# Optimization experiments

Measured on AMD Instinct MI355X. Metric: run time of the kernel, lower is better.

The kernel has to match this reference:

```python
import jax, jax.numpy as jnp
import numpy as np

N = 8192        # num_nodes
H = 128         # h_dim
E = 131072      # num edges (avg degree 16)
NREL = 90       # num relations
NB = 8          # num_bases (block-diagonal decomposition)
SI = H // NB    # block size 16


def setup_inputs() -> dict:
    key = jax.random.key(0)
    ks = jax.random.split(key, 24)
    sc = 0.01
    n = lambda k, shape, s=sc: jax.random.normal(k, shape, dtype=jnp.float32) * s
    return {
        'node_ids': jnp.arange(N, dtype=jnp.int32),
        'src': jax.random.randint(ks[0], (E,), 0, N, dtype=jnp.int32),
        'dst': jax.random.randint(ks[1], (E,), 0, N, dtype=jnp.int32),
        'etypes': jax.random.randint(ks[2], (E,), 0, NREL, dtype=jnp.int32),
        'norm': jax.random.uniform(ks[3], (E, 1), dtype=jnp.float32),
        'eps': jax.random.normal(ks[4], (N, H), dtype=jnp.float32),
        # input embedding layer
        'embedding': n(ks[5], (N, H)),
        # RelGraphConv layer 0 ('bdd'): per-relation block-diag weights, self-loop, bias
        'W0': n(ks[6], (NREL, NB, SI, SI)),
        'loop0': n(ks[7], (H, H)),
        'b0': jnp.zeros((H,), jnp.float32),
        # RelGraphConv layer 1
        'W1': n(ks[8], (NREL, NB, SI, SI)),
        'loop1': n(ks[9], (H, H)),
        'b1': jnp.zeros((H,), jnp.float32),
        # z_layer: Linear(H, 2H)  (weights stored as (in, out))
        'Wz': n(ks[10], (H, 2 * H)),
        'bz': jnp.zeros((2 * H,), jnp.float32),
        # inter_layer (UpdateLayer): Linear(H, H) + h_bias
        'Wi': n(ks[11], (H, H)),
        'bi': jnp.zeros((H,), jnp.float32),
        'hbi': jnp.zeros((H,), jnp.float32),
        # output_layer (second UpdateLayer)
        'Wo': n(ks[12], (H, H)),
        'bo': jnp.zeros((H,), jnp.float32),
        'hbo': jnp.zeros((H,), jnp.float32),
    }


def _rgcn_bdd(h, W, loop_w, bias, src, dst, etypes, norm, act):
    # gather src features, split into NB blocks of size SI
    x = h[src].reshape(-1, NB, SI)                       # [E, NB, SI]
    Wg = W[etypes]                                       # [E, NB, SI, SI] per-edge relation block weights
    msg = jnp.einsum('ebi,ebio->ebo', x, Wg).reshape(-1, H) * norm  # [E, H]
    agg = jax.ops.segment_sum(msg, dst, num_segments=N)  # scatter-add to dst
    out = agg + bias + h @ loop_w                        # self-loop + bias
    return act(out) if act is not None else out


def reference(node_ids, src, dst, etypes, norm, eps, embedding,
              W0, loop0, b0, W1, loop1, b1,
              Wz, bz, Wi, bi, hbi, Wo, bo, hbo):
    # input layer: embedding lookup; saved as input_embed
    x0 = embedding[node_ids]                             # [N, H]
    h = _rgcn_bdd(x0, W0, loop0, b0, src, dst, etypes, norm, jax.nn.relu)
    h = _rgcn_bdd(h, W1, loop1, b1, src, dst, etypes, norm, None)
    # VAE head: z ~ N(mean, exp(log_std))
    zml = h @ Wz + bz                                    # [N, 2H]
    z_mean, z_log_std = jnp.split(zml, 2, axis=-1)
    z = z_mean + jnp.exp(z_log_std) * eps                # reparameterized sample
    # decode 1: outer-product reconstruction + fused update
    R = z @ z.T                                          # [N, N]
    h = R @ (z @ Wi + bi) + R @ x0 + hbi
    # decode 2
    R2 = h @ h.T                                         # [N, N]
    out = R2 @ (h @ Wo + bo) + R2 @ x0 + hbo
    return out
```

## Files before the change

### kernel.cpp

```cpp
#include <hip/hip_runtime.h>
#include <hip/hip_bf16.h>
#include <math.h>

#define Hdim 128
#define NBq 8
#define SIq 16

typedef __attribute__((ext_vector_type(8))) short short8x;
typedef __attribute__((ext_vector_type(4))) float f32x4;

__device__ inline unsigned short f2b(float f) {
  unsigned int u = __float_as_uint(f);
  return (unsigned short)((u + 0x7fffu + ((u >> 16) & 1u)) >> 16);
}
__device__ inline unsigned int pack2(float lo, float hi) {
  return (unsigned int)f2b(lo) | ((unsigned int)f2b(hi) << 16);
}

__global__ __launch_bounds__(256) void k_pre(
    const float* __restrict__ emb, const int* __restrict__ ids, float* __restrict__ x0,
    const float* __restrict__ W0, unsigned short* __restrict__ Wt0,
    const float* __restrict__ W1, unsigned short* __restrict__ Wt1, int w0elems,
    const float* __restrict__ l0, const float* __restrict__ l1,
    const float* __restrict__ Wi, const float* __restrict__ Wo, const float* __restrict__ Wz,
    unsigned short* __restrict__ l0t, unsigned short* __restrict__ l1t,
    unsigned short* __restrict__ Wit, unsigned short* __restrict__ Wot,
    unsigned short* __restrict__ Wzt,
    const int* __restrict__ dst, int* __restrict__ cnt, int E,
    int b1, int b2, int b3) {
  int bx = blockIdx.x, t = threadIdx.x;
  if (bx < b1) {
    int idx = bx * 256 + t;
    int n = idx >> 5, c4 = idx & 31;
    int s = ids[n];
    ((float4*)x0)[(size_t)n * 32 + c4] = ((const float4*)emb)[(size_t)s * 32 + c4];
  } else if (bx < b2) {
    int idx = (bx - b1) * 256 + t;
    const float* W = (idx < w0elems) ? W0 : W1;
    unsigned short* Wt = (idx < w0elems) ? Wt0 : Wt1;
    int local = (idx < w0elems) ? idx : idx - w0elems;
    int rb = local >> 8, io = local & 255;
    int i = io >> 4, o = io & 15;
    Wt[(size_t)rb * 256 + o * 16 + i] = f2b(W[(size_t)rb * 256 + i * 16 + o]);
  } else if (bx < b3) {
    int idx = (bx - b2) * 256 + t;
    if (idx < 65536) {
      int w = idx >> 14, local = idx & 16383;
      const float* in = (w == 0) ? l0 : (w == 1) ? l1 : (w == 2) ? Wi : Wo;
      unsigned short* out = (w == 0) ? l0t : (w == 1) ? l1t : (w == 2) ? Wit : Wot;
      int n = local >> 7, k = local & 127;
      out[local] = f2b(in[k * 128 + n]);
    } else {
      int local = idx - 65536;
      int n = local >> 7, k = local & 127;
      Wzt[local] = f2b(Wz[k * 256 + n]);
    }
  } else {
    int e = (bx - b3) * 256 + t;
    if (e < E) atomicAdd(&cnt[dst[e]], 1);
  }
}

__global__ __launch_bounds__(1024) void k_scan(const int* __restrict__ cnt,
                                               int* __restrict__ off,
                                               int* __restrict__ cur, int N, int E) {
  __shared__ int part[1024];
  int t = threadIdx.x;
  int ipt = N / 1024;
  int base = t * ipt;
  int loc[8];
  int s = 0;
  for (int i = 0; i < ipt; ++i) { loc[i] = s; s += cnt[base + i]; }
  part[t] = s;
  __syncthreads();
  for (int d = 1; d < 1024; d <<= 1) {
    int v = part[t];
    int add = (t >= d) ? part[t - d] : 0;
    __syncthreads();
    part[t] = v + add;
    __syncthreads();
  }
  int pre = (t == 0) ? 0 : part[t - 1];
  for (int i = 0; i < ipt; ++i) {
    int o = pre + loc[i];
    off[base + i] = o;
    cur[base + i] = o;
  }
  if (t == 0) off[N] = E;
}

__global__ void k_scatter(const int* __restrict__ src, const int* __restrict__ dst,
                          const int* __restrict__ et, const float* __restrict__ norm,
                          int* __restrict__ cur, int* __restrict__ psrc,
                          int* __restrict__ pet, float* __restrict__ pnorm, int E) {
  int e = blockIdx.x * blockDim.x + threadIdx.x;
  if (e >= E) return;
  int p = atomicAdd(&cur[dst[e]], 1);
  psrc[p] = src[e];
  pet[p]  = et[e];
  pnorm[p] = norm[e];
}

#define BF_LO(u) __uint_as_float((u) << 16)
#define BF_HI(u) __uint_as_float((u) & 0xffff0000u)

__device__ inline float edge_dot(const unsigned short* __restrict__ Wt,
                                 int r, int b, int o, const float* __restrict__ xrow) {
  const uint4* wp = (const uint4*)(Wt + ((size_t)r * NBq + b) * 256 + o * 16);
  uint4 wa = wp[0], wb = wp[1];
  const float4* xp = (const float4*)xrow;
  float4 x0 = xp[0], x1 = xp[1], x2 = xp[2], x3 = xp[3];
  return x0.x*BF_LO(wa.x) + x0.y*BF_HI(wa.x) + x0.z*BF_LO(wa.y) + x0.w*BF_HI(wa.y)
       + x1.x*BF_LO(wa.z) + x1.y*BF_HI(wa.z) + x1.z*BF_LO(wa.w) + x1.w*BF_HI(wa.w)
       + x2.x*BF_LO(wb.x) + x2.y*BF_HI(wb.x) + x2.z*BF_LO(wb.y) + x2.w*BF_HI(wb.y)
       + x3.x*BF_LO(wb.z) + x3.y*BF_HI(wb.z) + x3.z*BF_LO(wb.w) + x3.w*BF_HI(wb.w);
}

__global__ __launch_bounds__(128) void k_edge8(
    const float* __restrict__ h, const unsigned short* __restrict__ Wt,
    const int* __restrict__ off, const int* __restrict__ psrc,
    const int* __restrict__ pet, const float* __restrict__ pnorm,
    float* __restrict__ agg) {
  int n = blockIdx.x;
  int f = threadIdx.x;
  int b = f >> 4, o = f & 15;
  int j0 = off[n], j1 = off[n + 1];
  __shared__ float xs[8][Hdim];
  float acc = 0.f;
  for (int j = j0; j < j1; j += 8) {
    int m = j1 - j;
    if (m >= 8) {
#pragma unroll
      for (int q = 0; q < 8; ++q)
        xs[q][f] = h[(size_t)psrc[j + q] * Hdim + f];
      __syncthreads();
#pragma unroll
      for (int q = 0; q < 8; ++q) {
        int r = pet[j + q];
        float nv = pnorm[j + q];
        acc = fmaf(edge_dot(Wt, r, b, o, &xs[q][b * SIq]), nv, acc);
      }
      __syncthreads();
    } else {
      for (int q = 0; q < m; ++q)
        xs[q][f] = h[(size_t)psrc[j + q] * Hdim + f];
      __syncthreads();
      for (int q = 0; q < m; ++q) {
        int r = pet[j + q];
        float nv = pnorm[j + q];
        acc = fmaf(edge_dot(Wt, r, b, o, &xs[q][b * SIq]), nv, acc);
      }
      __syncthreads();
    }
  }
  agg[(size_t)n * Hdim + f] = acc;
}

__global__ __launch_bounds__(256) void k_bgemm(
    const float* __restrict__ A, const unsigned short* __restrict__ Bt,
    const float* __restrict__ Gsrc, float* __restrict__ C,
    const float* __restrict__ addm, const float* __restrict__ bias,
    int M, int Nc, int relu, float* __restrict__ gzero) {
  __shared__ unsigned short Al[32][136];
  __shared__ unsigned short Bl[64][136];
  int t = threadIdx.x;
  int bm = blockIdx.x * 32, bn = blockIdx.y * 64;
  if (gzero && blockIdx.x == 0 && blockIdx.y == 0) {
#pragma unroll
    for (int i = 0; i < 16; ++i)
      ((float4*)gzero)[t + 256 * i] = make_float4(0.f, 0.f, 0.f, 0.f);
  }
  {
    int r = t >> 3, c0 = (t & 7) << 4;
    const float4* ap = (const float4*)(A + (size_t)(bm + r) * Hdim + c0);
    float4 a0 = ap[0], a1 = ap[1], a2 = ap[2], a3 = ap[3];
    uint4 p0 = { pack2(a0.x, a0.y), pack2(a0.z, a0.w), pack2(a1.x, a1.y), pack2(a1.z, a1.w) };
    uint4 p1 = { pack2(a2.x, a2.y), pack2(a2.z, a2.w), pack2(a3.x, a3.y), pack2(a3.z, a3.w) };
    *(uint4*)&Al[r][c0]     = p0;
    *(uint4*)&Al[r][c0 + 8] = p1;
  }
  if (Bt) {
    int n = t >> 2, k0 = (t & 3) << 5;
    const uint4* bp = (const uint4*)(Bt + (size_t)(bn + n) * Hdim + k0);
    uint4 b0 = bp[0], b1 = bp[1], b2 = bp[2], b3 = bp[3];
    *(uint4*)&Bl[n][k0]      = b0;
    *(uint4*)&Bl[n][k0 + 8]  = b1;
    *(uint4*)&Bl[n][k0 + 16] = b2;
    *(uint4*)&Bl[n][k0 + 24] = b3;
  } else {
    int n = t & 63, kb = (t >> 6) << 5;
    for (int i = 0; i < 32; ++i) {
      int k = kb + i;
      Bl[n][k] = f2b(Gsrc[(size_t)k * 128 + bn + n]);
    }
  }
  __syncthreads();
  int wv = t >> 6, ln = t & 63;
  int mt = wv & 1;
  int nt0 = (wv >> 1) << 1;
  int lm = ln & 15, lk = ln >> 4;
  f32x4 acc0 = {0.f, 0.f, 0.f, 0.f}, acc1 = {0.f, 0.f, 0.f, 0.f};
#pragma unroll
  for (int ks = 0; ks < 4; ++ks) {
    short8x af = *(const short8x*)&Al[mt * 16 + lm][ks * 32 + lk * 8];
    short8x bf0 = *(const short8x*)&Bl[nt0 * 16 + lm][ks * 32 + lk * 8];
    short8x bf1 = *(const short8x*)&Bl[(nt0 + 1) * 16 + lm][ks * 32 + lk * 8];
    acc0 = __builtin_amdgcn_mfma_f32_16x16x32_bf16(af, bf0, acc0, 0, 0, 0);
    acc1 = __builtin_amdgcn_mfma_f32_16x16x32_bf16(af, bf1, acc1, 0, 0, 0);
  }
  int gcol0 = bn + nt0 * 16 + lm;
  int gcol1 = gcol0 + 16;
  float b0v = bias ? bias[gcol0] : 0.f;
  float b1v = bias ? bias[gcol1] : 0.f;
#pragma unroll
  for (int reg = 0; reg < 4; ++reg) {
    int grow = bm + mt * 16 + lk * 4 + reg;
    size_t o0 = (size_t)grow * Nc + gcol0;
    size_t o1 = (size_t)grow * Nc + gcol1;
    float v0 = acc0[reg] + b0v;
    float v1 = acc1[reg] + b1v;
    if (addm) { v0 += addm[o0]; v1 += addm[o1]; }
    if (relu) { v0 = fmaxf(v0, 0.f); v1 = fmaxf(v1, 0.f); }
    C[o0] = v0;
    C[o1] = v1;
  }
}

__global__ __launch_bounds__(256) void k_bgemm_z(
    const float* __restrict__ A, const unsigned short* __restrict__ Wzt,
    const float* __restrict__ bz, const float* __restrict__ eps,
    float* __restrict__ Z, int M) {
  __shared__ unsigned short Al[32][136];
  __shared__ unsigned short Bm[64][136];
  __shared__ unsigned short Bl[64][136];
  int t = threadIdx.x;
  int bm = blockIdx.x * 32, bn = blockIdx.y * 64;
  {
    int r = t >> 3, c0 = (t & 7) << 4;
    const float4* ap = (const float4*)(A + (size_t)(bm + r) * Hdim + c0);
    float4 a0 = ap[0], a1 = ap[1], a2 = ap[2], a3 = ap[3];
    uint4 p0 = { pack2(a0.x, a0.y), pack2(a0.z, a0.w), pack2(a1.x, a1.y), pack2(a1.z, a1.w) };
    uint4 p1 = { pack2(a2.x, a2.y), pack2(a2.z, a2.w), pack2(a3.x, a3.y), pack2(a3.z, a3.w) };
    *(uint4*)&Al[r][c0]     = p0;
    *(uint4*)&Al[r][c0 + 8] = p1;
  }
  {
    int n = t >> 2, k0 = (t & 3) << 5;
    const uint4* mp = (const uint4*)(Wzt + (size_t)(bn + n) * Hdim + k0);
    const uint4* lp = (const uint4*)(Wzt + (size_t)(bn + 128 + n) * Hdim + k0);
    uint4 m0 = mp[0], m1 = mp[1], m2 = mp[2], m3 = mp[3];
    uint4 l0 = lp[0], l1 = lp[1], l2 = lp[2], l3 = lp[3];
    *(uint4*)&Bm[n][k0]      = m0; *(uint4*)&Bm[n][k0 + 8]  = m1;
    *(uint4*)&Bm[n][k0 + 16] = m2; *(uint4*)&Bm[n][k0 + 24] = m3;
    *(uint4*)&Bl[n][k0]      = l0; *(uint4*)&Bl[n][k0 + 8]  = l1;
    *(uint4*)&Bl[n][k0 + 16] = l2; *(uint4*)&Bl[n][k0 + 24] = l3;
  }
  __syncthreads();
  int wv = t >> 6, ln = t & 63;
  int mt = wv & 1;
  int nt0 = (wv >> 1) << 1;
  int lm = ln & 15, lk = ln >> 4;
  f32x4 am0 = {0,0,0,0}, am1 = {0,0,0,0}, al0 = {0,0,0,0}, al1 = {0,0,0,0};
#pragma unroll
  for (int ks = 0; ks < 4; ++ks) {
    short8x af = *(const short8x*)&Al[mt * 16 + lm][ks * 32 + lk * 8];
    short8x bm0 = *(const short8x*)&Bm[nt0 * 16 + lm][ks * 32 + lk * 8];
    short8x bm1 = *(const short8x*)&Bm[(nt0 + 1) * 16 + lm][ks * 32 + lk * 8];
    short8x bl0 = *(const short8x*)&Bl[nt0 * 16 + lm][ks * 32 + lk * 8];
    short8x bl1 = *(const short8x*)&Bl[(nt0 + 1) * 16 + lm][ks * 32 + lk * 8];
    am0 = __builtin_amdgcn_mfma_f32_16x16x32_bf16(af, bm0, am0, 0, 0, 0);
    am1 = __builtin_amdgcn_mfma_f32_16x16x32_bf16(af, bm1, am1, 0, 0, 0);
    al0 = __builtin_amdgcn_mfma_f32_16x16x32_bf16(af, bl0, al0, 0, 0, 0);
    al1 = __builtin_amdgcn_mfma_f32_16x16x32_bf16(af, bl1, al1, 0, 0, 0);
  }
  int gcol0 = bn + nt0 * 16 + lm;
  int gcol1 = gcol0 + 16;
  float bm0v = bz[gcol0], bm1v = bz[gcol1];
  float bl0v = bz[128 + gcol0], bl1v = bz[128 + gcol1];
#pragma unroll
  for (int reg = 0; reg < 4; ++reg) {
    int grow = bm + mt * 16 + lk * 4 + reg;
    size_t o0 = (size_t)grow * Hdim + gcol0;
    size_t o1 = (size_t)grow * Hdim + gcol1;
    Z[o0] = am0[reg] + bm0v + expf(al0[reg] + bl0v) * eps[o0];
    Z[o1] = am1[reg] + bm1v + expf(al1[reg] + bl1v) * eps[o1];
  }
}

__global__ __launch_bounds__(256) void k_xty(const float* __restrict__ X,
                                             const float* __restrict__ Y,
                                             float* __restrict__ G, int N) {
  __shared__ float xs[8][64];
  __shared__ float ys[8][64];
  int t  = threadIdx.x;
  int tx = t & 15, ty = t >> 4;
  int qr = blockIdx.y >> 1, qc = blockIdx.y & 1;
  int KC = N / gridDim.x;
  int k0 = blockIdx.x * KC;
  int m  = t >> 7, li = t & 127;
  int lr = li >> 4, lc = (li & 15) << 2;
  const float* S = m ? Y : X;
  int coff = (m ? qc : qr) * 64;
  float acc[4][4] = {};
  for (int kb = 0; kb < KC; kb += 8) {
    float4 v = *(const float4*)(S + (size_t)(k0 + kb + lr) * Hdim + coff + lc);
    __syncthreads();
    if (m) *(float4*)&ys[lr][lc] = v; else *(float4*)&xs[lr][lc] = v;
    __syncthreads();
#pragma unroll
    for (int kk = 0; kk < 8; ++kk) {
      float4 xv = *(const float4*)&xs[kk][ty << 2];
      float4 yv = *(const float4*)&ys[kk][tx << 2];
      acc[0][0] += xv.x * yv.x; acc[0][1] += xv.x * yv.y; acc[0][2] += xv.x * yv.z; acc[0][3] += xv.x * yv.w;
      acc[1][0] += xv.y * yv.x; acc[1][1] += xv.y * yv.y; acc[1][2] += xv.y * yv.z; acc[1][3] += xv.y * yv.w;
      acc[2][0] += xv.z * yv.x; acc[2][1] += xv.z * yv.y; acc[2][2] += xv.z * yv.z; acc[2][3] += xv.z * yv.w;
      acc[3][0] += xv.w * yv.x; acc[3][1] += xv.w * yv.y; acc[3][2] += xv.w * yv.z; acc[3][3] += xv.w * yv.w;
    }
  }
  int grow = qr * 64 + (ty << 2);
  int gcol = qc * 64 + (tx << 2);
#pragma unroll
  for (int r = 0; r < 4; ++r)
#pragma unroll
    for (int c = 0; c < 4; ++c)
      atomicAdd(&G[(size_t)(grow + r) * Hdim + gcol + c], acc[r][c]);
}

extern "C" void kernel_launch(void* const* d_in, const int* in_sizes, int n_in,
                              void* d_out, int out_size, void* d_ws, size_t ws_size,
                              hipStream_t stream) {
  const int*   node_ids = (const int*)d_in[0];
  const int*   src      = (const int*)d_in[1];
  const int*   dst      = (const int*)d_in[2];
  const int*   et       = (const int*)d_in[3];
  const float* norm     = (const float*)d_in[4];
  const float* eps      = (const float*)d_in[5];
  const float* emb      = (const float*)d_in[6];
  const float* W0       = (const float*)d_in[7];
  const float* loop0    = (const float*)d_in[8];
  const float* b0       = (const float*)d_in[9];
  const float* W1       = (const float*)d_in[10];
  const float* loop1    = (const float*)d_in[11];
  const float* b1       = (const float*)d_in[12];
  const float* Wz       = (const float*)d_in[13];
  const float* bz       = (const float*)d_in[14];
  const float* Wi       = (const float*)d_in[15];
  const float* bi       = (const float*)d_in[16];
  const float* hbi      = (const float*)d_in[17];
  const float* Wo       = (const float*)d_in[18];
  const float* bo       = (const float*)d_in[19];
  const float* hbo      = (const float*)d_in[20];
  float* out = (float*)d_out;

  const int N  = in_sizes[0];
  const int E  = in_sizes[1];
  const int RB = in_sizes[7] / (SIq * SIq);

  char* ws = (char*)d_ws;
  const size_t MB = 1u << 20;
  const size_t KB = 1u << 10;
  float* X0   = (float*)(ws + 0 * MB);
  float* B1p  = (float*)(ws + 4 * MB);
  float* B2p  = (float*)(ws + 8 * MB);
  float* AGG  = (float*)(ws + 12 * MB);
  float* B3p  = (float*)(ws + 16 * MB);
  float* G    = (float*)(ws + 20 * MB);
  int*   offp = (int*)(ws + 20 * MB + 256 * KB);
  int*   curp = (int*)(ws + 20 * MB + 512 * KB);
  int*   cntp = (int*)(ws + 20 * MB + 768 * KB);
  int*   psrc = (int*)(ws + 21 * MB);
  int*   pet  = (int*)(ws + 21 * MB + 512 * KB);
  float* pnrm = (float*)(ws + 22 * MB);
  unsigned short* Wt0 = (unsigned short*)(ws + 22 * MB + 512 * KB);
  unsigned short* Wt1 = (unsigned short*)(ws + 23 * MB);
  unsigned short* l0t = (unsigned short*)(ws + 24 * MB);
  unsigned short* l1t = (unsigned short*)(ws + 24 * MB + 64 * KB);
  unsigned short* Wit = (unsigned short*)(ws + 24 * MB + 128 * KB);
  unsigned short* Wot = (unsigned short*)(ws + 24 * MB + 192 * KB);
  unsigned short* Wzt = (unsigned short*)(ws + 24 * MB + 256 * KB);

  dim3 blk(256);

  const int w0elems = RB * 256;
  const int gB   = (N * 32) / 256;
  const int wtbB = (2 * w0elems + 255) / 256;
  const int wttB = 98304 / 256;
  const int histB = (E + 255) / 256;
  const int b1s = gB, b2s = gB + wtbB, b3s = gB + wtbB + wttB;
  hipMemsetAsync(cntp, 0, (size_t)N * sizeof(int), stream);
  k_pre<<<dim3(b3s + histB), blk, 0, stream>>>(
      emb, node_ids, X0, W0, Wt0, W1, Wt1, w0elems,
      loop0, loop1, Wi, Wo, Wz, l0t, l1t, Wit, Wot, Wzt,
      dst, cntp, E, b1s, b2s, b3s);
  k_scan<<<dim3(1), dim3(1024), 0, stream>>>(cntp, offp, curp, N, E);
  k_scatter<<<dim3((E + 255) / 256), blk, 0, stream>>>(src, dst, et, norm, curp,
                                                       psrc, pet, pnrm, E);

  k_edge8<<<dim3(N), dim3(128), 0, stream>>>(X0, Wt0, offp, psrc, pet, pnrm, AGG);
  k_bgemm<<<dim3(N / 32, 2), blk, 0, stream>>>(X0, l0t, nullptr, B1p, AGG, b0, N, Hdim, 1, nullptr);
  k_edge8<<<dim3(N), dim3(128), 0, stream>>>(B1p, Wt1, offp, psrc, pet, pnrm, AGG);
  k_bgemm<<<dim3(N / 32, 2), blk, 0, stream>>>(B1p, l1t, nullptr, B2p, AGG, b1, N, Hdim, 0, nullptr);
  k_bgemm_z<<<dim3(N / 32, 2), blk, 0, stream>>>(B2p, Wzt, bz, eps, B1p, N);
  k_bgemm<<<dim3(N / 32, 2), blk, 0, stream>>>(B1p, Wit, nullptr, B3p, X0, bi, N, Hdim, 0, G);
  k_xty<<<dim3(32, 4), blk, 0, stream>>>(B1p, B3p, G, N);
  k_bgemm<<<dim3(N / 32, 2), blk, 0, stream>>>(B1p, nullptr, G, B2p, nullptr, hbi, N, Hdim, 0, nullptr);
  k_bgemm<<<dim3(N / 32, 2), blk, 0, stream>>>(B2p, Wot, nullptr, B3p, X0, bo, N, Hdim, 0, G);
  k_xty<<<dim3(32, 4), blk, 0, stream>>>(B2p, B3p, G, N);
  k_bgemm<<<dim3(N / 32, 2), blk, 0, stream>>>(B2p, nullptr, G, out, nullptr, hbo, N, Hdim, 0, nullptr);
}
```

Baseline: 285.9 us.

## Gather fp16 node features in edge kernel with fdot2, drop LDS staging

Node features for the two RGCN message-passing layers are now also written as fp16 copies, one in the embedding gather and one in the layer-0 GEMM epilogue. Relation block weights are stored as fp16 instead of bf16. The edge kernel now loads each neighbor's 16-element fp16 slice directly from global memory and uses packed fp16 dot-product instructions, with no shared-memory staging or barriers. The aim is to halve gather bandwidth and remove sync overhead, at the cost of extra fp16 stores and reduced precision on inputs and weights.

```diff
diff --git a/kernel.cpp b/kernel.cpp
--- a/kernel.cpp
+++ b/kernel.cpp
@@ -8,6 +8,8 @@
 
 typedef __attribute__((ext_vector_type(8))) short short8x;
 typedef __attribute__((ext_vector_type(4))) float f32x4;
+typedef __attribute__((ext_vector_type(4))) unsigned short ushort4x;
+typedef __attribute__((ext_vector_type(2))) _Float16 half2x;
 
 __device__ inline unsigned short f2b(float f) {
   unsigned int u = __float_as_uint(f);
@@ -16,9 +18,21 @@
 __device__ inline unsigned int pack2(float lo, float hi) {
   return (unsigned int)f2b(lo) | ((unsigned int)f2b(hi) << 16);
 }
+__device__ inline unsigned short f2h(float f) {
+  _Float16 h = (_Float16)f;
+  unsigned short u;
+  __builtin_memcpy(&u, &h, 2);
+  return u;
+}
+__device__ inline half2x u2h(unsigned int u) {
+  union { unsigned int u; half2x h; } v;
+  v.u = u;
+  return v.h;
+}
 
 __global__ __launch_bounds__(256) void k_pre(
     const float* __restrict__ emb, const int* __restrict__ ids, float* __restrict__ x0,
+    unsigned short* __restrict__ x0h,
     const float* __restrict__ W0, unsigned short* __restrict__ Wt0,
     const float* __restrict__ W1, unsigned short* __restrict__ Wt1, int w0elems,
     const float* __restrict__ l0, const float* __restrict__ l1,
@@ -33,7 +47,11 @@
     int idx = bx * 256 + t;
     int n = idx >> 5, c4 = idx & 31;
     int s = ids[n];
-    ((float4*)x0)[(size_t)n * 32 + c4] = ((const float4*)emb)[(size_t)s * 32 + c4];
+    float4 v = ((const float4*)emb)[(size_t)s * 32 + c4];
+    ((float4*)x0)[(size_t)n * 32 + c4] = v;
+    ushort4x h;
+    h.x = f2h(v.x); h.y = f2h(v.y); h.z = f2h(v.z); h.w = f2h(v.w);
+    ((ushort4x*)x0h)[(size_t)n * 32 + c4] = h;
   } else if (bx < b2) {
     int idx = (bx - b1) * 256 + t;
     const float* W = (idx < w0elems) ? W0 : W1;
@@ -41,7 +59,7 @@
     int local = (idx < w0elems) ? idx : idx - w0elems;
     int rb = local >> 8, io = local & 255;
     int i = io >> 4, o = io & 15;
-    Wt[(size_t)rb * 256 + o * 16 + i] = f2b(W[(size_t)rb * 256 + i * 16 + o]);
+    Wt[(size_t)rb * 256 + o * 16 + i] = f2h(W[(size_t)rb * 256 + i * 16 + o]);
   } else if (bx < b3) {
     int idx = (bx - b2) * 256 + t;
     if (idx < 65536) {
@@ -101,23 +119,8 @@
   pnorm[p] = norm[e];
 }
 
-#define BF_LO(u) __uint_as_float((u) << 16)
-#define BF_HI(u) __uint_as_float((u) & 0xffff0000u)
-
-__device__ inline float edge_dot(const unsigned short* __restrict__ Wt,
-                                 int r, int b, int o, const float* __restrict__ xrow) {
-  const uint4* wp = (const uint4*)(Wt + ((size_t)r * NBq + b) * 256 + o * 16);
-  uint4 wa = wp[0], wb = wp[1];
-  const float4* xp = (const float4*)xrow;
-  float4 x0 = xp[0], x1 = xp[1], x2 = xp[2], x3 = xp[3];
-  return x0.x*BF_LO(wa.x) + x0.y*BF_HI(wa.x) + x0.z*BF_LO(wa.y) + x0.w*BF_HI(wa.y)
-       + x1.x*BF_LO(wa.z) + x1.y*BF_HI(wa.z) + x1.z*BF_LO(wa.w) + x1.w*BF_HI(wa.w)
-       + x2.x*BF_LO(wb.x) + x2.y*BF_HI(wb.x) + x2.z*BF_LO(wb.y) + x2.w*BF_HI(wb.y)
-       + x3.x*BF_LO(wb.z) + x3.y*BF_HI(wb.z) + x3.z*BF_LO(wb.w) + x3.w*BF_HI(wb.w);
-}
-
-__global__ __launch_bounds__(128) void k_edge8(
-    const float* __restrict__ h, const unsigned short* __restrict__ Wt,
+__global__ __launch_bounds__(128) void k_edge(
+    const unsigned short* __restrict__ xh, const unsigned short* __restrict__ Wt,
     const int* __restrict__ off, const int* __restrict__ psrc,
     const int* __restrict__ pet, const float* __restrict__ pnorm,
     float* __restrict__ agg) {
@@ -125,33 +128,38 @@
   int f = threadIdx.x;
   int b = f >> 4, o = f & 15;
   int j0 = off[n], j1 = off[n + 1];
-  __shared__ float xs[8][Hdim];
   float acc = 0.f;
-  for (int j = j0; j < j1; j += 8) {
-    int m = j1 - j;
-    if (m >= 8) {
-#pragma unroll
-      for (int q = 0; q < 8; ++q)
-        xs[q][f] = h[(size_t)psrc[j + q] * Hdim + f];
-      __syncthreads();
-#pragma unroll
-      for (int q = 0; q < 8; ++q) {
-        int r = pet[j + q];
-        float nv = pnorm[j + q];
-        acc = fmaf(edge_dot(Wt, r, b, o, &xs[q][b * SIq]), nv, acc);
-      }
-      __syncthreads();
-    } else {
-      for (int q = 0; q < m; ++q)
-        xs[q][f] = h[(size_t)psrc[j + q] * Hdim + f];
-      __syncthreads();
-      for (int q = 0; q < m; ++q) {
-        int r = pet[j + q];
-        float nv = pnorm[j + q];
-        acc = fmaf(edge_dot(Wt, r, b, o, &xs[q][b * SIq]), nv, acc);
-      }
-      __syncthreads();
+#pragma unroll 2
+  for (int j = j0; j < j1; ++j) {
+    int s = psrc[j];
+    int r = pet[j];
+    float nv = pnorm[j];
+    const uint4* xp = (const uint4*)(xh + (size_t)s * Hdim + b * SIq);
+    const uint4* wp = (const uint4*)(Wt + ((size_t)r * NBq + b) * 256 + o * SIq);
+    uint4 xa = xp[0], xc = xp[1];
+    uint4 wa = wp[0], wc = wp[1];
+#if __has_builtin(__builtin_amdgcn_fdot2)
+    float d0 = 0.f, d1 = 0.f;
+    d0 = __builtin_amdgcn_fdot2(u2h(xa.x), u2h(wa.x), d0, false);
+    d1 = __builtin_amdgcn_fdot2(u2h(xa.y), u2h(wa.y), d1, false);
+    d0 = __builtin_amdgcn_fdot2(u2h(xa.z), u2h(wa.z), d0, false);
+    d1 = __builtin_amdgcn_fdot2(u2h(xa.w), u2h(wa.w), d1, false);
+    d0 = __builtin_amdgcn_fdot2(u2h(xc.x), u2h(wc.x), d0, false);
+    d1 = __builtin_amdgcn_fdot2(u2h(xc.y), u2h(wc.y), d1, false);
+    d0 = __builtin_amdgcn_fdot2(u2h(xc.z), u2h(wc.z), d0, false);
+    d1 = __builtin_amdgcn_fdot2(u2h(xc.w), u2h(wc.w), d1, false);
+    acc = fmaf(d0 + d1, nv, acc);
+#else
+    float d = 0.f;
+    unsigned int xu[8] = {xa.x, xa.y, xa.z, xa.w, xc.x, xc.y, xc.z, xc.w};
+    unsigned int wu[8] = {wa.x, wa.y, wa.z, wa.w, wc.x, wc.y, wc.z, wc.w};
+#pragma unroll
+    for (int k = 0; k < 8; ++k) {
+      half2x xv = u2h(xu[k]), wv = u2h(wu[k]);
+      d += (float)xv.x * (float)wv.x + (float)xv.y * (float)wv.y;
     }
+    acc = fmaf(d, nv, acc);
+#endif
   }
   agg[(size_t)n * Hdim + f] = acc;
 }
@@ -160,7 +168,8 @@
     const float* __restrict__ A, const unsigned short* __restrict__ Bt,
     const float* __restrict__ Gsrc, float* __restrict__ C,
     const float* __restrict__ addm, const float* __restrict__ bias,
-    int M, int Nc, int relu, float* __restrict__ gzero) {
+    int M, int Nc, int relu, float* __restrict__ gzero,
+    unsigned short* __restrict__ Ch) {
   __shared__ unsigned short Al[32][136];
   __shared__ unsigned short Bl[64][136];
   int t = threadIdx.x;
@@ -223,6 +232,7 @@
     if (relu) { v0 = fmaxf(v0, 0.f); v1 = fmaxf(v1, 0.f); }
     C[o0] = v0;
     C[o1] = v1;
+    if (Ch) { Ch[o0] = f2h(v0); Ch[o1] = f2h(v1); }
   }
 }
 
@@ -378,6 +388,8 @@
   unsigned short* Wit = (unsigned short*)(ws + 24 * MB + 128 * KB);
   unsigned short* Wot = (unsigned short*)(ws + 24 * MB + 192 * KB);
   unsigned short* Wzt = (unsigned short*)(ws + 24 * MB + 256 * KB);
+  unsigned short* X0H = (unsigned short*)(ws + 25 * MB);
+  unsigned short* B1H = (unsigned short*)(ws + 27 * MB);
 
   dim3 blk(256);
 
@@ -389,22 +401,22 @@
   const int b1s = gB, b2s = gB + wtbB, b3s = gB + wtbB + wttB;
   hipMemsetAsync(cntp, 0, (size_t)N * sizeof(int), stream);
   k_pre<<<dim3(b3s + histB), blk, 0, stream>>>(
-      emb, node_ids, X0, W0, Wt0, W1, Wt1, w0elems,
+      emb, node_ids, X0, X0H, W0, Wt0, W1, Wt1, w0elems,
       loop0, loop1, Wi, Wo, Wz, l0t, l1t, Wit, Wot, Wzt,
       dst, cntp, E, b1s, b2s, b3s);
   k_scan<<<dim3(1), dim3(1024), 0, stream>>>(cntp, offp, curp, N, E);
   k_scatter<<<dim3((E + 255) / 256), blk, 0, stream>>>(src, dst, et, norm, curp,
                                                        psrc, pet, pnrm, E);
 
-  k_edge8<<<dim3(N), dim3(128), 0, stream>>>(X0, Wt0, offp, psrc, pet, pnrm, AGG);
-  k_bgemm<<<dim3(N / 32, 2), blk, 0, stream>>>(X0, l0t, nullptr, B1p, AGG, b0, N, Hdim, 1, nullptr);
-  k_edge8<<<dim3(N), dim3(128), 0, stream>>>(B1p, Wt1, offp, psrc, pet, pnrm, AGG);
-  k_bgemm<<<dim3(N / 32, 2), blk, 0, stream>>>(B1p, l1t, nullptr, B2p, AGG, b1, N, Hdim, 0, nullptr);
+  k_edge<<<dim3(N), dim3(128), 0, stream>>>(X0H, Wt0, offp, psrc, pet, pnrm, AGG);
+  k_bgemm<<<dim3(N / 32, 2), blk, 0, stream>>>(X0, l0t, nullptr, B1p, AGG, b0, N, Hdim, 1, nullptr, B1H);
+  k_edge<<<dim3(N), dim3(128), 0, stream>>>(B1H, Wt1, offp, psrc, pet, pnrm, AGG);
+  k_bgemm<<<dim3(N / 32, 2), blk, 0, stream>>>(B1p, l1t, nullptr, B2p, AGG, b1, N, Hdim, 0, nullptr, nullptr);
   k_bgemm_z<<<dim3(N / 32, 2), blk, 0, stream>>>(B2p, Wzt, bz, eps, B1p, N);
-  k_bgemm<<<dim3(N / 32, 2), blk, 0, stream>>>(B1p, Wit, nullptr, B3p, X0, bi, N, Hdim, 0, G);
+  k_bgemm<<<dim3(N / 32, 2), blk, 0, stream>>>(B1p, Wit, nullptr, B3p, X0, bi, N, Hdim, 0, G, nullptr);
   k_xty<<<dim3(32, 4), blk, 0, stream>>>(B1p, B3p, G, N);
-  k_bgemm<<<dim3(N / 32, 2), blk, 0, stream>>>(B1p, nullptr, G, B2p, nullptr, hbi, N, Hdim, 0, nullptr);
-  k_bgemm<<<dim3(N / 32, 2), blk, 0, stream>>>(B2p, Wot, nullptr, B3p, X0, bo, N, Hdim, 0, G);
+  k_bgemm<<<dim3(N / 32, 2), blk, 0, stream>>>(B1p, nullptr, G, B2p, nullptr, hbi, N, Hdim, 0, nullptr, nullptr);
+  k_bgemm<<<dim3(N / 32, 2), blk, 0, stream>>>(B2p, Wot, nullptr, B3p, X0, bo, N, Hdim, 0, G, nullptr);
   k_xty<<<dim3(32, 4), blk, 0, stream>>>(B2p, B3p, G, N);
-  k_bgemm<<<dim3(N / 32, 2), blk, 0, stream>>>(B2p, nullptr, G, out, nullptr, hbo, N, Hdim, 0, nullptr);
-}
+  k_bgemm<<<dim3(N / 32, 2), blk, 0, stream>>>(B2p, nullptr, G, out, nullptr, hbo, N, Hdim, 0, nullptr, nullptr);
+}
```

Result: slower. 297.2 us (+4.0%).
